# Kernel tuning notes

Measured on AMD Instinct MI355X. Metric: run time of the kernel, lower is better.

The kernel has to match this reference:

```python
import jax, jax.numpy as jnp
import numpy as np

OBS_DIM = 1024
HEADS = 16
SCALE = OBS_DIM ** (-0.5)  # note: full obs_dim, as in the original module


def setup_inputs() -> dict:
    key = jax.random.key(0)
    k1, k2, k3, k4 = jax.random.split(key, 4)
    x = jax.random.normal(k1, (4, 2048, OBS_DIM), dtype=jnp.float32)
    # torch nn.Linear weight layout: [out_features, in_features]
    w_qkv = jax.random.normal(k2, (3 * OBS_DIM, OBS_DIM), dtype=jnp.float32) * (OBS_DIM ** -0.5)
    w_out = jax.random.normal(k3, (OBS_DIM, OBS_DIM), dtype=jnp.float32) * (OBS_DIM ** -0.5)
    b_out = jax.random.normal(k4, (OBS_DIM,), dtype=jnp.float32) * 0.02
    return {"x": x, "w_qkv": w_qkv, "w_out": w_out, "b_out": b_out}


def reference(x, w_qkv, w_out, b_out):
    b, n, dm = x.shape
    h = HEADS
    d = dm // h
    qkv = x @ w_qkv.T  # [b, n, 3*dm]
    # rearrange 'b n (c h d) -> c b h n d'
    qkv = qkv.reshape(b, n, 3, h, d)
    q = jnp.transpose(qkv[:, :, 0], (0, 2, 1, 3))  # [b,h,n,d]
    k = jnp.transpose(qkv[:, :, 1], (0, 2, 1, 3))
    v = jnp.transpose(qkv[:, :, 2], (0, 2, 1, 3))
    scores = jnp.einsum('bhid,bhjd->bhij', q, k) * SCALE
    att = jax.nn.softmax(scores, axis=-1)
    ctx = jnp.einsum('bhij,bhjd->bhid', att, v)  # [b,h,n,d]
    ctx = jnp.transpose(ctx, (0, 2, 1, 3)).reshape(b, n, dm)
    return ctx @ w_out.T + b_out
```

## Files before the change

kernel.cpp:

```cpp
#include <hip/hip_runtime.h>
#include <hip/hip_bf16.h>


typedef __attribute__((ext_vector_type(8))) short short8;
typedef __attribute__((ext_vector_type(4))) float float4x;
typedef __attribute__((ext_vector_type(2))) unsigned uint2x;

#define QS 8388608

#if __has_builtin(__builtin_amdgcn_exp2f)
#define FASTEXP(x) __builtin_amdgcn_exp2f(x)
#define QPRESCALE 0.0450842203f
#else
#define FASTEXP(x) __expf(x)
#define QPRESCALE 0.03125f
#endif

static __device__ __forceinline__ float4x mfma32(short8 a, short8 b, float4x c) {
    return __builtin_amdgcn_mfma_f32_16x16x32_bf16(a, b, c, 0, 0, 0);
}

static __device__ __forceinline__ void pl32swap(unsigned &a, unsigned &b) {
#if __has_builtin(__builtin_amdgcn_permlane32_swap)
    uint2x r = __builtin_amdgcn_permlane32_swap(a, b, false, false);
    a = r[0]; b = r[1];
#else
    asm("v_permlane32_swap_b32 %0, %1" : "+v"(a), "+v"(b));
#endif
}
static __device__ __forceinline__ void pl16swap(unsigned &a, unsigned &b) {
#if __has_builtin(__builtin_amdgcn_permlane16_swap)
    uint2x r = __builtin_amdgcn_permlane16_swap(a, b, false, false);
    a = r[0]; b = r[1];
#else
    asm("v_permlane16_swap_b32 %0, %1" : "+v"(a), "+v"(b));
#endif
}

static __device__ __forceinline__ short f2bf(float f) {
    union { float f; unsigned u; } x; x.f = f;
    unsigned r = x.u + 0x7fffu + ((x.u >> 16) & 1u);
    return (short)(r >> 16);
}
static __device__ __forceinline__ unsigned pack2(float a, float b) {
    return (unsigned)(unsigned short)f2bf(a) | ((unsigned)(unsigned short)f2bf(b) << 16);
}
static __device__ __forceinline__ unsigned fbits(float f) {
    union { float f; unsigned u; } x; x.f = f; return x.u;
}
static __device__ __forceinline__ unsigned permpack(float lo, float hi) {
    return __builtin_amdgcn_perm(fbits(hi), fbits(lo), 0x07060302u);
}
static __device__ __forceinline__ void async16(const void* g, void* l) {
    __builtin_amdgcn_global_load_lds(
        (const __attribute__((address_space(1))) void*)g,
        (__attribute__((address_space(3))) void*)l, 16, 0, 0);
}

__global__ __launch_bounds__(256) void cast_kernel(
    const float* __restrict__ x, const float* __restrict__ wq, const float* __restrict__ wo,
    short* __restrict__ xo, short* __restrict__ wqo, short* __restrict__ woo)
{
    int i = blockIdx.x * 256 + threadIdx.x;
    const float* src; short* dst; int off;
    if (i < 2097152)      { src = x;  dst = xo;  off = i; }
    else if (i < 2883584) { src = wq; dst = wqo; off = i - 2097152; }
    else                  { src = wo; dst = woo; off = i - 2883584; }
    float4 v = *(const float4*)(src + (size_t)off * 4);
    unsigned t[2] = {pack2(v.x, v.y), pack2(v.z, v.w)};
    *(uint2*)(dst + (size_t)off * 4) = *(uint2*)t;
}

template<int MODE>
__global__ __launch_bounds__(256) void gemm_bt_kernel(
    const short* __restrict__ A, const short* __restrict__ W,
    const float* __restrict__ bias, void* __restrict__ outp,
    int M, int N, int K)
{
    __shared__ short sh[32768];
    short* const A0 = sh;
    short* const W0 = sh + 8192;
    short* const A1 = sh + 16384;
    short* const W1 = sh + 24576;

    const int tid  = threadIdx.x;
    const int lane = tid & 63;
    const int wave = tid >> 6;
    const int row16 = lane & 15;
    const int quad  = lane >> 4;
    const int wm = wave >> 1, wn = wave & 1;

    const int l  = blockIdx.y * 64 + blockIdx.x;
    const int xcd = l & 7, s = l >> 3;
    const int m0 = (xcd * 8 + (s & 7)) * 128;
    const int n0 = (s >> 3) * 128;

    float4x acc[4][4] = {};

    auto stageAW = [&](int kb, short* Ad, short* Wd) {
        for (int r = 0; r < 4; r++) {
            int i = r * 256 + tid, row = i >> 3, cc = i & 7, sc = cc ^ (row & 7);
            async16(A + (size_t)(m0 + row) * K + kb + sc * 8, Ad + i * 8);
        }
        for (int r = 0; r < 4; r++) {
            int i = r * 256 + tid, row = i >> 3, cc = i & 7, sc = cc ^ (row & 7);
            async16(W + (size_t)(n0 + row) * K + kb + sc * 8, Wd + i * 8);
        }
    };

    stageAW(0, A0, W0);
    __syncthreads();
    const int KI = K >> 6;
    for (int ki = 0; ki < KI; ki++) {
        short* const Ac = (ki & 1) ? A1 : A0;
        short* const Wc = (ki & 1) ? W1 : W0;
        short* const An = (ki & 1) ? A0 : A1;
        short* const Wn = (ki & 1) ? W0 : W1;
        if (ki + 1 < KI) stageAW((ki + 1) << 6, An, Wn);

        short8 af[4][2], bfr[4][2];
        for (int mt = 0; mt < 4; mt++)
            for (int h = 0; h < 2; h++) {
                int row = wm * 64 + mt * 16 + row16;
                af[mt][h] = *(const short8*)&Ac[row * 64 + (((h << 2) | quad) ^ (row & 7)) * 8];
            }
        for (int nt = 0; nt < 4; nt++)
            for (int h = 0; h < 2; h++) {
                int row = wn * 64 + nt * 16 + row16;
                bfr[nt][h] = *(const short8*)&Wc[row * 64 + (((h << 2) | quad) ^ (row & 7)) * 8];
            }
        for (int mt = 0; mt < 4; mt++)
            for (int nt = 0; nt < 4; nt++) {
                acc[mt][nt] = __builtin_amdgcn_mfma_f32_16x16x32_bf16(af[mt][0], bfr[nt][0], acc[mt][nt], 0, 0, 0);
                acc[mt][nt] = __builtin_amdgcn_mfma_f32_16x16x32_bf16(af[mt][1], bfr[nt][1], acc[mt][nt], 0, 0, 0);
            }
        __syncthreads();
    }

    if (MODE == 0) {
        for (int mt = 0; mt < 4; mt++)
            for (int nt = 0; nt < 4; nt++)
                for (int r = 0; r < 4; r++) {
                    int mm = m0 + wm * 64 + mt * 16 + quad * 4 + r;
                    int nn = n0 + wn * 64 + nt * 16 + row16;
                    ((float*)outp)[(size_t)mm * N + nn] = acc[mt][nt][r] + bias[nn];
                }
    } else {
        const int c  = n0 >> 10;
        const int bb = m0 >> 11;
        for (int nt = 0; nt < 4; nt++) {
            const int rem = (n0 & 1023) + wn * 64 + nt * 16 + row16;
            const int hh = rem >> 6, dd = rem & 63;
            for (int mt = 0; mt < 4; mt++) {
                const int nsq0 = (m0 & 2047) + wm * 64 + mt * 16 + quad * 4;
                if (c == 2) {
                    size_t off = 2 * (size_t)QS + (((size_t)(bb * 16 + hh) * 64 + dd) * 2048 + nsq0);
                    uint2 w;
                    w.x = pack2(acc[mt][nt][0], acc[mt][nt][1]);
                    w.y = pack2(acc[mt][nt][2], acc[mt][nt][3]);
                    *(uint2*)((short*)outp + off) = w;
                } else {
                    size_t off = (size_t)c * QS + (((size_t)(bb * 16 + hh) * 2048 + nsq0) * 64 + dd);
                    const float scl = (c == 0) ? QPRESCALE : 1.f;
                    for (int r = 0; r < 4; r++)
                        ((short*)outp)[off + (size_t)r * 64] = f2bf(acc[mt][nt][r] * scl);
                }
            }
        }
    }
}

__global__ __launch_bounds__(256, 3) void flash_kernel(
    const short* __restrict__ Q, const short* __restrict__ Km,
    const short* __restrict__ VT, short* __restrict__ ctx)
{
    __shared__ __align__(16) short sh[16384];

    const int id = blockIdx.y * 8 + blockIdx.x;
    const int bh = ((id & 7) << 3) | ((id >> 3) & 7);
    const int qt = id >> 6;

    const int tid  = threadIdx.x;
    const int wave = tid >> 6;
    const int lane = tid & 63;
    const int row16 = lane & 15;
    const int quad  = lane >> 4;
    const size_t basekq = (size_t)bh * 2048 * 64;
    const size_t basev  = (size_t)bh * 64 * 2048;

    short* const bufA = sh;
    short* const bufB = sh + 8192;

    short8 q[2][2];
    {
        const int qrow0 = qt * 128 + wave * 32 + row16;
        for (int u = 0; u < 2; u++)
            for (int h = 0; h < 2; h++)
                q[u][h] = *(const short8*)(Q + basekq
                            + (size_t)(qrow0 + u * 16) * 64 + (size_t)(((h << 2) | quad)) * 8);
    }

    const int srow = tid >> 3;
    const int ssc  = ((tid & 7) ^ (srow & 7)) * 8;
    const short* gk  = Km + basekq + (size_t)srow * 64 + ssc;
    const short* gk2 = gk + 2048;
    const short* gv  = VT + basev + (size_t)srow * 2048 + ssc;
    const short* gv2 = gv + 65536;
    const int ldst = tid * 8;

    const int koff0 = row16 * 64 + ((quad ^ (row16 & 7))) * 8;
    const int koff1 = row16 * 64 + (((4 | quad) ^ (row16 & 7))) * 8;

    async16(gk,  bufB + ldst);        async16(gk2, bufB + ldst + 2048);
    async16(gv,  bufB + 4096 + ldst); async16(gv2, bufB + 4096 + ldst + 2048);
    gk += 4096; gk2 += 4096; gv += 64; gv2 += 64;
    __syncthreads();

    float4x accO[2][4] = {};
    float lsum[2] = {0.f, 0.f};
    const float4x FZ = {};

    for (int kt = 0; kt < 32; kt++) {
        short* const cur = (kt & 1) ? bufA : bufB;
        short* const nxt = (kt & 1) ? bufB : bufA;
        if (kt < 31) {
            async16(gk,  nxt + ldst);        async16(gk2, nxt + ldst + 2048);
            async16(gv,  nxt + 4096 + ldst); async16(gv2, nxt + 4096 + ldst + 2048);
            gk += 4096; gk2 += 4096; gv += 64; gv2 += 64;
        }

        const short* b0 = cur + koff0;
        const short* b1 = cur + koff1;

        float4x sfA[4], sfB[4];
        {
            short8 kf[4][2];
#pragma unroll
            for (int jt = 0; jt < 4; jt++) {
                kf[jt][0] = *(const short8*)(b0 + jt * 1024);
                kf[jt][1] = *(const short8*)(b1 + jt * 1024);
            }
            __builtin_amdgcn_s_setprio(1);
#pragma unroll
            for (int jt = 0; jt < 4; jt++) {
                float4x s0 = mfma32(kf[jt][0], q[0][0], FZ);
                sfA[jt] = mfma32(kf[jt][1], q[0][1], s0);
            }
#pragma unroll
            for (int jt = 0; jt < 4; jt++) {
                float4x s0 = mfma32(kf[jt][0], q[1][0], FZ);
                sfB[jt] = mfma32(kf[jt][1], q[1][1], s0);
            }
            __builtin_amdgcn_s_setprio(0);
        }

        short8 vf[4][2];
#pragma unroll
        for (int jt = 0; jt < 4; jt++) {
            vf[jt][0] = *(const short8*)(b0 + 4096 + jt * 1024);
            vf[jt][1] = *(const short8*)(b1 + 4096 + jt * 1024);
        }

        auto smpv = [&](float4x (&sf)[4], float4x (&aO)[4], float &ls) {
            short8 pf[2];
#pragma unroll
            for (int jp = 0; jp < 2; jp++) {
                float4x sa = sf[jp * 2], sb = sf[jp * 2 + 1];
                float a0 = FASTEXP(sa[0]), a1 = FASTEXP(sa[1]);
                float a2 = FASTEXP(sa[2]), a3 = FASTEXP(sa[3]);
                float b0e = FASTEXP(sb[0]), b1e = FASTEXP(sb[1]);
                float b2e = FASTEXP(sb[2]), b3e = FASTEXP(sb[3]);
                ls += ((a0 + a1) + (a2 + a3)) + ((b0e + b1e) + (b2e + b3e));
                unsigned wa0 = permpack(a0, a1), wa1 = permpack(a2, a3);
                unsigned wb0 = permpack(b0e, b1e), wb1 = permpack(b2e, b3e);
                pl32swap(wa0, wb0); pl16swap(wa0, wb0);
                pl32swap(wa1, wb1); pl16swap(wa1, wb1);
                union { unsigned w[4]; short8 s; } pk;
                pk.w[0] = wa0; pk.w[1] = wa1; pk.w[2] = wb0; pk.w[3] = wb1;
                pf[jp] = pk.s;
            }
            __builtin_amdgcn_s_setprio(1);
#pragma unroll
            for (int dt = 0; dt < 4; dt++) {
                aO[dt] = mfma32(vf[dt][0], pf[0], aO[dt]);
                aO[dt] = mfma32(vf[dt][1], pf[1], aO[dt]);
            }
            __builtin_amdgcn_s_setprio(0);
        };
        smpv(sfA, accO[0], lsum[0]);
        smpv(sfB, accO[1], lsum[1]);

        __syncthreads();
    }

    const int bb = bh >> 4, hh = bh & 15;
    for (int u = 0; u < 2; u++) {
        float l = lsum[u];
        l += __shfl_xor(l, 16);
        l += __shfl_xor(l, 32);
        const float inv = 1.f / l;
        const int nrow = qt * 128 + wave * 32 + u * 16 + row16;
        for (int dt = 0; dt < 4; dt++) {
            uint2 w;
            w.x = pack2(accO[u][dt][0] * inv, accO[u][dt][1] * inv);
            w.y = pack2(accO[u][dt][2] * inv, accO[u][dt][3] * inv);
            *(uint2*)(ctx + (size_t)(bb * 2048 + nrow) * 1024 + hh * 64 + dt * 16 + quad * 4) = w;
        }
    }
}

extern "C" void kernel_launch(void* const* d_in, const int* in_sizes, int n_in,
                              void* d_out, int out_size, void* d_ws, size_t ws_size,
                              hipStream_t stream) {
    const float* x     = (const float*)d_in[0];
    const float* w_qkv = (const float*)d_in[1];
    const float* w_out = (const float*)d_in[2];
    const float* b_out = (const float*)d_in[3];
    float* out = (float*)d_out;
    short* ws  = (short*)d_ws;

    short* qkv_ws  = ws;
    short* xbf     = ws + (size_t)3 * QS;
    short* ctx_ws  = xbf;
    short* wqkv_bf = ws + (size_t)4 * QS;
    short* wout_bf = wqkv_bf + 3145728;

    dim3 blk(256);
    cast_kernel<<<12288, blk, 0, stream>>>(x, w_qkv, w_out, xbf, wqkv_bf, wout_bf);
    gemm_bt_kernel<1><<<dim3(64, 24), blk, 0, stream>>>(xbf, wqkv_bf, nullptr, qkv_ws,
                                                        8192, 3072, 1024);
    flash_kernel<<<dim3(8, 128), blk, 0, stream>>>(qkv_ws, qkv_ws + QS, qkv_ws + 2 * (size_t)QS,
                                                   ctx_ws);
    gemm_bt_kernel<0><<<dim3(64, 8), blk, 0, stream>>>(ctx_ws, wout_bf, b_out, out,
                                                       8192, 1024, 1024);
}
```

Measured before the change: 244.4 us.

## Add 256x256-tile 8-wave QKV GEMM with interleaved async loads

Replaces the QKV projection GEMM with a new kernel that uses 256x256 output tiles, 512 threads (8 waves), double-buffered 128KB LDS filled by global_load_lds, and loads staged between MFMA quarter-blocks with s_setprio. A swizzled block index improves L2 locality. The larger tile raises arithmetic intensity and the interleaving hides load latency, at the cost of occupancy (one block per CU from LDS) and only 384 blocks for 256 CUs, which leaves a tail wave.

```diff
diff --git a/kernel.cpp b/kernel.cpp
--- a/kernel.cpp
+++ b/kernel.cpp
@@ -56,6 +56,8 @@
         (const __attribute__((address_space(1))) void*)g,
         (__attribute__((address_space(3))) void*)l, 16, 0, 0);
 }
+
+#define GBAR() asm volatile("s_barrier" ::: "memory")
 
 __global__ __launch_bounds__(256) void cast_kernel(
     const float* __restrict__ x, const float* __restrict__ wq, const float* __restrict__ wo,
@@ -69,6 +71,139 @@
     float4 v = *(const float4*)(src + (size_t)off * 4);
     unsigned t[2] = {pack2(v.x, v.y), pack2(v.z, v.w)};
     *(uint2*)(dst + (size_t)off * 4) = *(uint2*)t;
+}
+
+#define QUADS(mh, nh) \
+    __builtin_amdgcn_s_setprio(1); \
+    _Pragma("unroll") \
+    for (int mt_ = 0; mt_ < 4; mt_++) { \
+        _Pragma("unroll") \
+        for (int nt_ = 0; nt_ < 2; nt_++) { \
+            acc[(mh)*4+mt_][(nh)*2+nt_] = mfma32(af[mt_][0], bf[(nh)*2+nt_][0], acc[(mh)*4+mt_][(nh)*2+nt_]); \
+            acc[(mh)*4+mt_][(nh)*2+nt_] = mfma32(af[mt_][1], bf[(nh)*2+nt_][1], acc[(mh)*4+mt_][(nh)*2+nt_]); \
+        } \
+    } \
+    __builtin_amdgcn_s_setprio(0)
+
+__global__ __launch_bounds__(512) void gemm_qkv256_kernel(
+    const short* __restrict__ A, const short* __restrict__ W,
+    short* __restrict__ outp, int M, int N, int K)
+{
+    __shared__ __align__(16) short sh[65536];
+
+    const int tid   = threadIdx.x;
+    const int lane  = tid & 63;
+    const int wave  = tid >> 6;
+    const int wm    = wave >> 2;
+    const int wn    = wave & 3;
+    const int row16 = lane & 15;
+    const int quad  = lane >> 4;
+
+    const int l   = blockIdx.x;
+    const int swz = (l & 7) * 48 + (l >> 3);
+    const int m0  = (swz / 12) * 256;
+    const int n0  = (swz % 12) * 256;
+
+    const int riu = tid >> 3;
+    const int ssc = ((tid & 7) ^ (riu & 7)) * 8;
+    const short* pA = A + (size_t)(m0 + riu) * K + ssc;
+    const short* pB = W + (size_t)(n0 + riu) * K + ssc;
+    const size_t us = (size_t)64 * K;
+    short* const d0 = sh + tid * 8;
+
+    const int koff0 = row16 * 64 + ((quad ^ (row16 & 7))) * 8;
+    const int koff1 = row16 * 64 + (((4 | quad) ^ (row16 & 7))) * 8;
+
+#pragma unroll
+    for (int u = 0; u < 4; u++) async16(pA + u * us,      d0 + u * 4096);
+#pragma unroll
+    for (int u = 0; u < 4; u++) async16(pB + u * us,      d0 + 16384 + u * 4096);
+#pragma unroll
+    for (int u = 0; u < 4; u++) async16(pA + u * us + 64, d0 + 32768 + u * 4096);
+#pragma unroll
+    for (int u = 0; u < 4; u++) async16(pB + u * us + 64, d0 + 49152 + u * 4096);
+    asm volatile("s_waitcnt vmcnt(8)" ::: "memory");
+    GBAR();
+
+    float4x acc[8][4] = {};
+
+    const int KI = K >> 6;
+    for (int kt = 0; kt < KI; kt++) {
+        const short* const cbuf = sh + (kt & 1) * 32768;
+        const short* const aB = cbuf + wm * 8192;
+        const short* const bB = cbuf + 16384 + wn * 4096;
+        short* const dst2 = d0 + (kt & 1) * 32768;
+        const int  kb2 = (kt + 2) << 6;
+        const bool st  = (kt + 2) < KI;
+
+        short8 bf[4][2], af[4][2];
+#pragma unroll
+        for (int nt = 0; nt < 4; nt++) {
+            bf[nt][0] = *(const short8*)(bB + nt * 1024 + koff0);
+            bf[nt][1] = *(const short8*)(bB + nt * 1024 + koff1);
+        }
+#pragma unroll
+        for (int mt = 0; mt < 4; mt++) {
+            af[mt][0] = *(const short8*)(aB + mt * 1024 + koff0);
+            af[mt][1] = *(const short8*)(aB + mt * 1024 + koff1);
+        }
+        GBAR();
+        QUADS(0, 0);
+        GBAR();
+        if (st) {
+#pragma unroll
+            for (int u = 0; u < 4; u++) async16(pB + u * us + kb2, dst2 + 16384 + u * 4096);
+        }
+        GBAR();
+        QUADS(0, 1);
+        GBAR();
+#pragma unroll
+        for (int mt = 0; mt < 4; mt++) {
+            af[mt][0] = *(const short8*)(aB + 4096 + mt * 1024 + koff0);
+            af[mt][1] = *(const short8*)(aB + 4096 + mt * 1024 + koff1);
+        }
+        if (st) {
+            async16(pA + 0 * us + kb2, dst2 + 0 * 4096);
+            async16(pA + 2 * us + kb2, dst2 + 2 * 4096);
+        }
+        GBAR();
+        QUADS(1, 0);
+        GBAR();
+        if (st) {
+            async16(pA + 1 * us + kb2, dst2 + 1 * 4096);
+            async16(pA + 3 * us + kb2, dst2 + 3 * 4096);
+        }
+        GBAR();
+        QUADS(1, 1);
+        if (st) asm volatile("s_waitcnt vmcnt(8)" ::: "memory");
+        else    asm volatile("s_waitcnt vmcnt(0)" ::: "memory");
+        GBAR();
+    }
+
+    const int c  = n0 >> 10;
+    const int bb = m0 >> 11;
+#pragma unroll
+    for (int nt = 0; nt < 4; nt++) {
+        const int rem = (n0 & 1023) + wn * 64 + nt * 16 + row16;
+        const int hh = rem >> 6, dd = rem & 63;
+#pragma unroll
+        for (int mt = 0; mt < 8; mt++) {
+            const int nsq0 = (m0 & 2047) + wm * 128 + mt * 16 + quad * 4;
+            if (c == 2) {
+                size_t off = 2 * (size_t)QS + (((size_t)(bb * 16 + hh) * 64 + dd) * 2048 + nsq0);
+                uint2 w;
+                w.x = pack2(acc[mt][nt][0], acc[mt][nt][1]);
+                w.y = pack2(acc[mt][nt][2], acc[mt][nt][3]);
+                *(uint2*)(outp + off) = w;
+            } else {
+                size_t off = (size_t)c * QS + (((size_t)(bb * 16 + hh) * 2048 + nsq0) * 64 + dd);
+                const float scl = (c == 0) ? QPRESCALE : 1.f;
+#pragma unroll
+                for (int r = 0; r < 4; r++)
+                    outp[off + (size_t)r * 64] = f2bf(acc[mt][nt][r] * scl);
+            }
+        }
+    }
 }
 
 template<int MODE>
@@ -327,8 +462,7 @@
 
     dim3 blk(256);
     cast_kernel<<<12288, blk, 0, stream>>>(x, w_qkv, w_out, xbf, wqkv_bf, wout_bf);
-    gemm_bt_kernel<1><<<dim3(64, 24), blk, 0, stream>>>(xbf, wqkv_bf, nullptr, qkv_ws,
-                                                        8192, 3072, 1024);
+    gemm_qkv256_kernel<<<384, 512, 0, stream>>>(xbf, wqkv_bf, qkv_ws, 8192, 3072, 1024);
     flash_kernel<<<dim3(8, 128), blk, 0, stream>>>(qkv_ws, qkv_ws + QS, qkv_ws + 2 * (size_t)QS,
                                                    ctx_ws);
     gemm_bt_kernel<0><<<dim3(64, 8), blk, 0, stream>>>(ctx_ws, wout_bf, b_out, out,
```

After: 270.8 us. +10.8%, slower.
